# Kernel tuning notes

Measured on AMD Instinct MI355X. Metric: run time of the kernel, lower is better.

Reference implementation:

```python
import jax, jax.numpy as jnp
import numpy as np

B, D, E, G, P, H = 8192, 2048, 8, 4, 512, 192
T, DT, TAU, VTH, VRESET = 20, 0.001, 0.02, 0.5, 0.0
DELTA0, KTOP, KROUTE, PREDW = 7.0, 32, 2, 0.1


def setup_inputs() -> dict:
    key = jax.random.key(0)
    ks = jax.random.split(key, 12)
    s = 0.02
    return {
        "query_embedding": jax.random.normal(ks[0], (B, D), jnp.float32),
        "Wg": jax.random.normal(ks[1], (2, E), jnp.float32) * s,
        "bg": jnp.zeros((E,), jnp.float32),
        "Wp": jax.random.normal(ks[2], (2, E), jnp.float32) * s,
        "bp": jnp.zeros((E,), jnp.float32),
        "Wgg": jax.random.normal(ks[3], (2, G), jnp.float32) * s,
        "bgg": jnp.zeros((G,), jnp.float32),
        "W1": jax.random.normal(ks[4], (E, D, P), jnp.float32) * (1.0 / np.sqrt(D)),
        "b1": jnp.zeros((E, P), jnp.float32),
        "W2": jax.random.normal(ks[5], (E, P, D), jnp.float32) * (1.0 / np.sqrt(P)),
        "b2": jnp.zeros((E, D), jnp.float32),
    }


def reference(query_embedding, Wg, bg, Wp, bp, Wgg, bgg, W1, b1, W2, b2):
    x = query_embedding  # [B, D], already embed_dim -> no pad/slice
    dtype = x.dtype

    # --- Phasor bank temporal features on per-row mean ---
    qm = jnp.mean(x, axis=-1)  # [B]
    freqs = DELTA0 * jnp.arange(1, H + 1, dtype=dtype)  # [H]
    ang = qm[:, None] * freqs[None, :]  # [B, H]
    temporal = jnp.concatenate([jnp.cos(ang), jnp.sin(ang)], axis=-1)  # [B, 2H]

    # --- Spiking attention over top-K |x| indices (LIF over T steps) ---
    topk_idx = jax.lax.top_k(jnp.abs(x), KTOP)[1]  # [B, K]
    rows = jnp.arange(B)[:, None]
    I = jnp.zeros((B, D), dtype).at[rows, topk_idx].add(1.0)  # input current [B, vocab=D]

    def lif_step(v, _):
        v = v * (1.0 - DT / TAU) + I
        spike = (v >= VTH).astype(dtype)
        v = jnp.where(spike > 0, VRESET, v)
        return v, spike

    _, spikes = jax.lax.scan(lif_step, jnp.zeros((B, D), dtype), None, length=T)
    attention_gains = jnp.mean(spikes, axis=0)  # [B, D] spike rates

    # --- Bio gating inputs ---
    gate_in = jnp.stack([jnp.mean(temporal, axis=-1), jnp.mean(attention_gains, axis=-1)], axis=-1)  # [B, 2]

    gate_logits = gate_in @ Wg + bg  # [B, E]
    gate_logits = gate_logits - PREDW * (gate_in @ Wp + bp)

    # group routing bias: experts grouped round-robin i % G
    group_logits = gate_in @ Wgg + bgg  # [B, G]
    gmap = jax.nn.one_hot(jnp.arange(E) % G, G, dtype=dtype)  # [E, G]
    gate_logits = gate_logits + group_logits @ gmap.T

    gate_weights = jax.nn.softmax(gate_logits, axis=-1)  # temperature = 1

    # top-k routing + renormalization
    _, tidx = jax.lax.top_k(gate_weights, KROUTE)
    mask = jnp.zeros_like(gate_weights).at[rows, tidx].set(1.0)
    gated = gate_weights * mask
    gate_weights = gated / (jnp.sum(gated, axis=-1, keepdims=True) + 1e-9)

    # --- Dense MLP experts (bottleneck P = hidden // 4) ---
    h = jax.nn.relu(jnp.einsum('bd,edp->ebp', x, W1) + b1[:, None, :])  # [E, B, P]
    expert_out = jnp.einsum('ebp,eph->ebh', h, W2) + b2[:, None, :]  # [E, B, D]

    # gate-weighted combine
    context = jnp.einsum('be,ebh->bh', gate_weights, expert_out)  # [B, D]
    return context
```

## Files before the change

### kernel.cpp

```cpp
#include <hip/hip_runtime.h>
#include <stdint.h>

#define NB 8192
#define ND 2048
#define NE 8
#define NG 4
#define NP 512
#define NH 192

typedef _Float16 half_t;
typedef half_t f16x8 __attribute__((ext_vector_type(8)));
typedef float f32x4 __attribute__((ext_vector_type(4)));

__device__ __forceinline__ void gload16(const void* g, void* l) {
  __builtin_amdgcn_global_load_lds(
      (const __attribute__((address_space(1))) void*)g,
      (__attribute__((address_space(3))) void*)l, 16, 0, 0);
}

__global__ __launch_bounds__(256) void k_convert(
    const float* __restrict__ x, half_t* __restrict__ xh, double* __restrict__ qm)
{
  const int b = blockIdx.x;
  const int t = threadIdx.x;
  const float* xr = x + (size_t)b * ND;
  const float4 v0 = ((const float4*)xr)[t * 2];
  const float4 v1 = ((const float4*)xr)[t * 2 + 1];
  float f[8] = {v0.x, v0.y, v0.z, v0.w, v1.x, v1.y, v1.z, v1.w};
  double s = 0.0;
  __align__(16) half_t hb[8];
#pragma unroll
  for (int i = 0; i < 8; i++) { s += (double)f[i]; hb[i] = (half_t)f[i]; }
  *reinterpret_cast<int4*>(xh + (size_t)b * ND + t * 8) = *reinterpret_cast<const int4*>(hb);

#pragma unroll
  for (int m = 32; m >= 1; m >>= 1) s += __shfl_xor(s, m);
  __shared__ double part[4];
  if ((t & 63) == 0) part[t >> 6] = s;
  __syncthreads();
  if (t == 0) qm[b] = (part[0] + part[1] + part[2] + part[3]) / (double)ND;
}

__global__ __launch_bounds__(256) void k_gate(
    const double* __restrict__ qm,
    const float* __restrict__ Wg, const float* __restrict__ bg,
    const float* __restrict__ Wp, const float* __restrict__ bp,
    const float* __restrict__ Wgg, const float* __restrict__ bgg,
    int* __restrict__ e0a, int* __restrict__ e1a,
    float* __restrict__ w0a, float* __restrict__ w1a)
{
  const int wave = threadIdx.x >> 6;
  const int lane = threadIdx.x & 63;
  const int b = blockIdx.x * 4 + wave;
  const double q = qm[b];

  double part = 0.0;
#pragma unroll
  for (int i = 0; i < 3; i++) {
    int h = lane + i * 64;
    double ang = q * (7.0 * (double)(h + 1));
    part += cos(ang) + sin(ang);
  }
#pragma unroll
  for (int m = 32; m >= 1; m >>= 1) part += __shfl_xor(part, m);
  const double tm = part / (2.0 * (double)NH);
  const double gi1 = 32.0 / 2048.0;

  double lg = -1.0e300;
  if (lane < 8) {
    const int e = lane, g = e & 3;
    lg = tm * (double)Wg[e] + gi1 * (double)Wg[NE + e] + (double)bg[e];
    lg -= 0.1 * (tm * (double)Wp[e] + gi1 * (double)Wp[NE + e] + (double)bp[e]);
    lg += tm * (double)Wgg[g] + gi1 * (double)Wgg[NG + g] + (double)bgg[g];
  }
  double mx = lg;
#pragma unroll
  for (int m = 4; m >= 1; m >>= 1) mx = fmax(mx, __shfl_xor(mx, m));
  double pe = 0.0;
  if (lane < 8) pe = exp(lg - mx);
  double ps = pe;
#pragma unroll
  for (int m = 4; m >= 1; m >>= 1) ps += __shfl_xor(ps, m);

  double lgs[8], pes[8];
#pragma unroll
  for (int e = 0; e < 8; e++) { lgs[e] = __shfl(lg, e); pes[e] = __shfl(pe, e); }

  if (lane == 0) {
    int e0 = 0;
    for (int e = 1; e < NE; e++) if (lgs[e] > lgs[e0]) e0 = e;
    int e1 = (e0 == 0) ? 1 : 0;
    for (int e = 0; e < NE; e++) if (e != e0 && lgs[e] > lgs[e1]) e1 = e;
    const double p0 = pes[e0] / ps;
    const double p1 = pes[e1] / ps;
    const double den = p0 + p1 + 1e-9;
    e0a[b] = e0; e1a[b] = e1;
    w0a[b] = (float)(p0 / den);
    w1a[b] = (float)(p1 / den);
  }
}

__global__ __launch_bounds__(256) void k_bucket(
    const int* __restrict__ e0a, const int* __restrict__ e1a,
    const float* __restrict__ w0a, const float* __restrict__ w1a,
    int* __restrict__ rowl, float* __restrict__ wl, int* __restrict__ cnt,
    int* __restrict__ pos0a, int* __restrict__ pos1a,
    int* __restrict__ rowlp, int* __restrict__ cntp)
{
  const int t = threadIdx.x;
  const int r = blockIdx.x * 256 + t;
  __shared__ int hist[16], base[16], cursor[16];
  __shared__ int histp[64], basep[64], cursorp[64];
  if (t < 16) { hist[t] = 0; cursor[t] = 0; }
  if (t < 64) { histp[t] = 0; cursorp[t] = 0; }
  __syncthreads();

  const int e0 = e0a[r], e1 = e1a[r];
  const int p = e0 * 8 + e1;
  atomicAdd(&hist[e0], 1);
  atomicAdd(&hist[8 + e1], 1);
  atomicAdd(&histp[p], 1);
  __syncthreads();
  if (t < 16) base[t] = atomicAdd(&cnt[t], hist[t]);
  if (t < 64) basep[t] = atomicAdd(&cntp[t], histp[t]);
  __syncthreads();

  int p0 = atomicAdd(&cursor[e0], 1);
  int idx0 = base[e0] + p0;
  rowl[e0 * NB + idx0] = r;
  wl[e0 * NB + idx0] = w0a[r];
  pos0a[r] = idx0;

  int p1 = atomicAdd(&cursor[8 + e1], 1);
  int idx1 = base[8 + e1] + p1;
  rowl[(8 + e1) * NB + idx1] = r;
  wl[(8 + e1) * NB + idx1] = w1a[r];
  pos1a[r] = idx1;

  int pp = atomicAdd(&cursorp[p], 1);
  rowlp[p * NB + basep[p] + pp] = r;
}

__global__ __launch_bounds__(256) void k_cvt_w(
    const float* __restrict__ W1, const float* __restrict__ W2,
    half_t* __restrict__ w1t, half_t* __restrict__ w2t)
{
  const int which = blockIdx.y;
  const int R = which ? NP : ND;
  const int C = which ? ND : NP;
  const float* src = which ? W2 : W1;
  half_t* dst = which ? w2t : w1t;
  const int tiles_c = C >> 5;
  const int tiles_per_e = (R >> 5) * tiles_c;
  int id = blockIdx.x;
  int e = id / tiles_per_e;
  int rem = id - e * tiles_per_e;
  int tr = rem / tiles_c, tc = rem - tr * tiles_c;
  __shared__ float tile[32][33];
  const int tx = threadIdx.x & 31, ty = threadIdx.x >> 5;
  const float* s = src + (size_t)e * R * C + (size_t)(tr * 32) * C + tc * 32;
#pragma unroll
  for (int i = 0; i < 4; i++)
    tile[ty + i * 8][tx] = s[(size_t)(ty + i * 8) * C + tx];
  __syncthreads();
  half_t* d = dst + (size_t)e * R * C + (size_t)(tc * 32) * R + tr * 32;
#pragma unroll
  for (int i = 0; i < 4; i++)
    d[(size_t)(ty + i * 8) * R + tx] = (half_t)tile[tx][ty + i * 8];
}

__global__ void k_prefix(const int* __restrict__ cnt, const int* __restrict__ cntp,
                         int* __restrict__ pbase,
                         int* __restrict__ i16b, int* __restrict__ i16m, int* __restrict__ n16,
                         int* __restrict__ ipp, int* __restrict__ ipm, int* __restrict__ np)
{
  if (threadIdx.x == 0 && blockIdx.x == 0) {
    int s = 0;
    for (int i = 0; i < 16; i++) { pbase[i] = s; s += cnt[i]; }
    int t = 0;
    for (int b = 0; b < 16; b++)
      for (int m0 = 0; m0 < cnt[b]; m0 += 128) { i16b[t] = b; i16m[t] = m0; t++; }
    *n16 = t;
    t = 0;
    for (int p = 0; p < 64; p++)
      for (int m0 = 0; m0 < cntp[p]; m0 += 128) { ipp[t] = p; ipm[t] = m0; t++; }
    *np = t;
  }
}

__global__ __launch_bounds__(256) void k_gemm1(
    const half_t* __restrict__ xh, const half_t* __restrict__ w1t,
    const float* __restrict__ b1,
    const int* __restrict__ rowl, const float* __restrict__ wl,
    const int* __restrict__ cnt, const int* __restrict__ pbase,
    const int* __restrict__ i16b, const int* __restrict__ i16m,
    const int* __restrict__ n16, half_t* __restrict__ Hbuf)
{
  const int wi = blockIdx.y;
  if (wi >= *n16) return;
  const int bucket = i16b[wi];
  const int m0 = i16m[wi];
  const int count = cnt[bucket];
  const int e = bucket & 7;
  const int n0 = blockIdx.x * 128;
  const int t = threadIdx.x;

  __shared__ __align__(16) half_t As[128 * 32];
  __shared__ __align__(16) half_t Bs[128 * 32];
  __shared__ int rows_s[128];
  __shared__ float ws_s[128];

  if (t < 128) {
    int mi = m0 + t;
    int idx = bucket * NB + (mi < count ? mi : m0);
    rows_s[t] = rowl[idx];
    ws_s[t] = wl[idx];
  }
  __syncthreads();

  const int w = t >> 6, lane = t & 63;
  const int c0 = w * 128 + lane, c1 = c0 + 64;
  const half_t* gA0 = xh + (size_t)rows_s[c0 >> 2] * ND + (c0 & 3) * 8;
  const half_t* gA1 = xh + (size_t)rows_s[c1 >> 2] * ND + (c1 & 3) * 8;
  const half_t* w1te = w1t + (size_t)e * NP * ND;
  const half_t* gB0 = w1te + (size_t)(n0 + (c0 >> 2)) * ND + (c0 & 3) * 8;
  const half_t* gB1 = w1te + (size_t)(n0 + (c1 >> 2)) * ND + (c1 & 3) * 8;
  half_t* lA0 = As + (w * 128) * 8;
  half_t* lA1 = As + (w * 128 + 64) * 8;
  half_t* lB0 = Bs + (w * 128) * 8;
  half_t* lB1 = Bs + (w * 128 + 64) * 8;

  const int wr = w >> 1, wc = w & 1;
  const int lrow = lane & 15, lk = lane >> 4;

  f32x4 acc[4][4];
#pragma unroll
  for (int i = 0; i < 4; i++)
#pragma unroll
    for (int j = 0; j < 4; j++) {
      acc[i][j][0] = 0.f; acc[i][j][1] = 0.f; acc[i][j][2] = 0.f; acc[i][j][3] = 0.f;
    }

  for (int k0 = 0; k0 < ND; k0 += 32) {
    gload16(gA0 + k0, lA0);
    gload16(gA1 + k0, lA1);
    gload16(gB0 + k0, lB0);
    gload16(gB1 + k0, lB1);
    __syncthreads();
    f16x8 af[4], bf[4];
#pragma unroll
    for (int i = 0; i < 4; i++) {
      af[i] = *reinterpret_cast<const f16x8*>(&As[(wr * 64 + i * 16 + lrow) * 32 + lk * 8]);
      bf[i] = *reinterpret_cast<const f16x8*>(&Bs[(wc * 64 + i * 16 + lrow) * 32 + lk * 8]);
    }
#pragma unroll
    for (int mi = 0; mi < 4; mi++)
#pragma unroll
      for (int ni = 0; ni < 4; ni++)
        acc[mi][ni] = __builtin_amdgcn_mfma_f32_16x16x32_f16(af[mi], bf[ni], acc[mi][ni], 0, 0, 0);
    __syncthreads();
  }

  const int pb = pbase[bucket];
#pragma unroll
  for (int mi = 0; mi < 4; mi++) {
#pragma unroll
    for (int i = 0; i < 4; i++) {
      int lm = wr * 64 + mi * 16 + lk * 4 + i;
      if (m0 + lm < count) {
        size_t prow = (size_t)(pb + m0 + lm) * NP;
        float wcoef = ws_s[lm];
#pragma unroll
        for (int ni = 0; ni < 4; ni++) {
          int col = n0 + wc * 64 + ni * 16 + lrow;
          float v = acc[mi][ni][i] + b1[e * NP + col];
          v = v > 0.f ? v : 0.f;
          Hbuf[prow + col] = (half_t)(v * wcoef);
        }
      }
    }
  }
}

__global__ __launch_bounds__(256) void k_gemm2p(
    const half_t* __restrict__ Hbuf, const half_t* __restrict__ w2t,
    const float* __restrict__ b2,
    const int* __restrict__ rowlp, const int* __restrict__ cntp,
    const int* __restrict__ pbase,
    const int* __restrict__ pos0a, const int* __restrict__ pos1a,
    const float* __restrict__ w0a, const float* __restrict__ w1a,
    const int* __restrict__ ipp, const int* __restrict__ ipm,
    const int* __restrict__ np, float* __restrict__ out)
{
  const int wi = blockIdx.y;
  if (wi >= *np) return;
  const int p = ipp[wi];
  const int m0 = ipm[wi];
  const int count = cntp[p];
  const int e0 = p >> 3, e1 = p & 7;
  const int n0 = blockIdx.x * 128;
  const int t = threadIdx.x;

  __shared__ __align__(16) half_t As[128 * 32];
  __shared__ __align__(16) half_t Bs[128 * 32];
  __shared__ int h0_s[128], h1_s[128], rs_s[128];
  __shared__ float w0_s[128], w1_s[128];

  if (t < 128) {
    int mi = m0 + t;
    int r = rowlp[p * NB + (mi < count ? mi : m0)];
    rs_s[t] = r;
    h0_s[t] = pbase[e0] + pos0a[r];
    h1_s[t] = pbase[8 + e1] + pos1a[r];
    w0_s[t] = w0a[r];
    w1_s[t] = w1a[r];
  }
  __syncthreads();

  const int w = t >> 6, lane = t & 63;
  const int c0 = w * 128 + lane, c1 = c0 + 64;
  const half_t* w2e0 = w2t + (size_t)e0 * ND * NP;
  const half_t* w2e1 = w2t + (size_t)e1 * ND * NP;
  const half_t* gB0e0 = w2e0 + (size_t)(n0 + (c0 >> 2)) * NP + (c0 & 3) * 8;
  const half_t* gB1e0 = w2e0 + (size_t)(n0 + (c1 >> 2)) * NP + (c1 & 3) * 8;
  const half_t* gB0e1 = w2e1 + (size_t)(n0 + (c0 >> 2)) * NP + (c0 & 3) * 8;
  const half_t* gB1e1 = w2e1 + (size_t)(n0 + (c1 >> 2)) * NP + (c1 & 3) * 8;
  const half_t* gA0s0 = Hbuf + (size_t)h0_s[c0 >> 2] * NP + (c0 & 3) * 8;
  const half_t* gA1s0 = Hbuf + (size_t)h0_s[c1 >> 2] * NP + (c1 & 3) * 8;
  const half_t* gA0s1 = Hbuf + (size_t)h1_s[c0 >> 2] * NP + (c0 & 3) * 8;
  const half_t* gA1s1 = Hbuf + (size_t)h1_s[c1 >> 2] * NP + (c1 & 3) * 8;
  half_t* lA0 = As + (w * 128) * 8;
  half_t* lA1 = As + (w * 128 + 64) * 8;
  half_t* lB0 = Bs + (w * 128) * 8;
  half_t* lB1 = Bs + (w * 128 + 64) * 8;

  const int wr = w >> 1, wc = w & 1;
  const int lrow = lane & 15, lk = lane >> 4;

  f32x4 acc[4][4];
#pragma unroll
  for (int i = 0; i < 4; i++)
#pragma unroll
    for (int j = 0; j < 4; j++) {
      acc[i][j][0] = 0.f; acc[i][j][1] = 0.f; acc[i][j][2] = 0.f; acc[i][j][3] = 0.f;
    }

  for (int k0 = 0; k0 < NP; k0 += 32) {
    gload16(gA0s0 + k0, lA0);
    gload16(gA1s0 + k0, lA1);
    gload16(gB0e0 + k0, lB0);
    gload16(gB1e0 + k0, lB1);
    __syncthreads();
    f16x8 af[4], bf[4];
#pragma unroll
    for (int i = 0; i < 4; i++) {
      af[i] = *reinterpret_cast<const f16x8*>(&As[(wr * 64 + i * 16 + lrow) * 32 + lk * 8]);
      bf[i] = *reinterpret_cast<const f16x8*>(&Bs[(wc * 64 + i * 16 + lrow) * 32 + lk * 8]);
    }
#pragma unroll
    for (int mi = 0; mi < 4; mi++)
#pragma unroll
      for (int ni = 0; ni < 4; ni++)
        acc[mi][ni] = __builtin_amdgcn_mfma_f32_16x16x32_f16(af[mi], bf[ni], acc[mi][ni], 0, 0, 0);
    __syncthreads();
  }
  for (int k0 = 0; k0 < NP; k0 += 32) {
    gload16(gA0s1 + k0, lA0);
    gload16(gA1s1 + k0, lA1);
    gload16(gB0e1 + k0, lB0);
    gload16(gB1e1 + k0, lB1);
    __syncthreads();
    f16x8 af[4], bf[4];
#pragma unroll
    for (int i = 0; i < 4; i++) {
      af[i] = *reinterpret_cast<const f16x8*>(&As[(wr * 64 + i * 16 + lrow) * 32 + lk * 8]);
      bf[i] = *reinterpret_cast<const f16x8*>(&Bs[(wc * 64 + i * 16 + lrow) * 32 + lk * 8]);
    }
#pragma unroll
    for (int mi = 0; mi < 4; mi++)
#pragma unroll
      for (int ni = 0; ni < 4; ni++)
        acc[mi][ni] = __builtin_amdgcn_mfma_f32_16x16x32_f16(af[mi], bf[ni], acc[mi][ni], 0, 0, 0);
    __syncthreads();
  }

  float b20[4], b21[4];
#pragma unroll
  for (int ni = 0; ni < 4; ni++) {
    int col = n0 + wc * 64 + ni * 16 + lrow;
    b20[ni] = b2[e0 * ND + col];
    b21[ni] = b2[e1 * ND + col];
  }
#pragma unroll
  for (int mi = 0; mi < 4; mi++) {
#pragma unroll
    for (int i = 0; i < 4; i++) {
      int lm = wr * 64 + mi * 16 + lk * 4 + i;
      if (m0 + lm < count) {
        int r = rs_s[lm];
        float wb0 = w0_s[lm], wb1 = w1_s[lm];
        float* orow = out + (size_t)r * ND;
#pragma unroll
        for (int ni = 0; ni < 4; ni++) {
          int col = n0 + wc * 64 + ni * 16 + lrow;
          orow[col] = acc[mi][ni][i] + wb0 * b20[ni] + wb1 * b21[ni];
        }
      }
    }
  }
}

extern "C" void kernel_launch(void* const* d_in, const int* in_sizes, int n_in,
                              void* d_out, int out_size, void* d_ws, size_t ws_size,
                              hipStream_t stream)
{
  const float* x   = (const float*)d_in[0];
  const float* Wg  = (const float*)d_in[1];
  const float* bg  = (const float*)d_in[2];
  const float* Wp  = (const float*)d_in[3];
  const float* bp  = (const float*)d_in[4];
  const float* Wgg = (const float*)d_in[5];
  const float* bgg = (const float*)d_in[6];
  const float* W1  = (const float*)d_in[7];
  const float* b1  = (const float*)d_in[8];
  const float* W2  = (const float*)d_in[9];
  const float* b2  = (const float*)d_in[10];
  float* out = (float*)d_out;

  char* ws = (char*)d_ws;
  size_t off = 0;
  const size_t OFF_XH   = off; off += (size_t)NB * ND * 2;
  const size_t OFF_W1T  = off; off += (size_t)NE * NP * ND * 2;
  const size_t OFF_W2T  = off; off += (size_t)NE * ND * NP * 2;
  const size_t OFF_H    = off; off += (size_t)(2 * NB + 128) * NP * 2;
  const size_t OFF_ROWL = off; off += (size_t)16 * NB * 4;
  const size_t OFF_WL   = off; off += (size_t)16 * NB * 4;
  const size_t OFF_ROWLP= off; off += (size_t)64 * NB * 4;
  const size_t OFF_CNT  = off; off += 64;
  const size_t OFF_CNTP = off; off += 256;
  const size_t OFF_PB   = off; off += 64;
  const size_t OFF_QM   = off; off += (size_t)NB * 8;
  const size_t OFF_E0   = off; off += (size_t)NB * 4;
  const size_t OFF_E1   = off; off += (size_t)NB * 4;
  const size_t OFF_W0   = off; off += (size_t)NB * 4;
  const size_t OFF_W1A  = off; off += (size_t)NB * 4;
  const size_t OFF_POS0 = off; off += (size_t)NB * 4;
  const size_t OFF_POS1 = off; off += (size_t)NB * 4;
  const size_t OFF_I16B = off; off += 1024;
  const size_t OFF_I16M = off; off += 1024;
  const size_t OFF_N16  = off; off += 64;
  const size_t OFF_IPP  = off; off += 1024;
  const size_t OFF_IPM  = off; off += 1024;
  const size_t OFF_NP   = off; off += 64;

  half_t* xh   = (half_t*)(ws + OFF_XH);
  half_t* w1t  = (half_t*)(ws + OFF_W1T);
  half_t* w2t  = (half_t*)(ws + OFF_W2T);
  half_t* Hbuf = (half_t*)(ws + OFF_H);
  int*    rowl = (int*)(ws + OFF_ROWL);
  float*  wl   = (float*)(ws + OFF_WL);
  int*    rowlp= (int*)(ws + OFF_ROWLP);
  int*    cnt  = (int*)(ws + OFF_CNT);
  int*    cntp = (int*)(ws + OFF_CNTP);
  int*    pb   = (int*)(ws + OFF_PB);
  double* qm   = (double*)(ws + OFF_QM);
  int*    e0a  = (int*)(ws + OFF_E0);
  int*    e1a  = (int*)(ws + OFF_E1);
  float*  w0a  = (float*)(ws + OFF_W0);
  float*  w1a  = (float*)(ws + OFF_W1A);
  int*    pos0a= (int*)(ws + OFF_POS0);
  int*    pos1a= (int*)(ws + OFF_POS1);
  int*    i16b = (int*)(ws + OFF_I16B);
  int*    i16m = (int*)(ws + OFF_I16M);
  int*    n16  = (int*)(ws + OFF_N16);
  int*    ipp  = (int*)(ws + OFF_IPP);
  int*    ipm  = (int*)(ws + OFF_IPM);
  int*    np   = (int*)(ws + OFF_NP);

  hipMemsetAsync(cnt, 0, 64 + 256, stream);
  k_convert<<<NB, 256, 0, stream>>>(x, xh, qm);
  k_cvt_w<<<dim3(8192, 2, 1), 256, 0, stream>>>(W1, W2, w1t, w2t);
  k_gate<<<NB / 4, 256, 0, stream>>>(qm, Wg, bg, Wp, bp, Wgg, bgg, e0a, e1a, w0a, w1a);
  k_bucket<<<NB / 256, 256, 0, stream>>>(e0a, e1a, w0a, w1a, rowl, wl, cnt,
                                         pos0a, pos1a, rowlp, cntp);
  k_prefix<<<1, 64, 0, stream>>>(cnt, cntp, pb, i16b, i16m, n16, ipp, ipm, np);
  k_gemm1<<<dim3(4, 144, 1), 256, 0, stream>>>(xh, w1t, b1, rowl, wl, cnt, pb,
                                               i16b, i16m, n16, Hbuf);
  k_gemm2p<<<dim3(16, 128, 1), 256, 0, stream>>>(Hbuf, w2t, b2, rowlp, cntp, pb,
                                                 pos0a, pos1a, w0a, w1a, ipp, ipm, np, out);
}
```

Before: 354.3 us.

## Triple-buffer LDS with async global_load_lds pipeline and XOR swizzle in expert GEMMs

Both grouped expert GEMM kernels now use a 3-stage LDS ring. Tiles are prefetched two iterations ahead with global_load_lds, and explicit vmcnt waits with a single barrier per step replace the two __syncthreads per step. The 16-byte chunks inside each 32-element row are XOR-swizzled by row to cut LDS bank conflicts on the fragment reads, and GEMM2's two expert loops are merged into one 32-step pipeline. In exchange, LDS use per block triples, which may lower occupancy, and the hand-written waitcnt sequencing must be exactly right.

```diff
diff --git a/kernel.cpp b/kernel.cpp
--- a/kernel.cpp
+++ b/kernel.cpp
@@ -205,8 +205,8 @@
   const int n0 = blockIdx.x * 128;
   const int t = threadIdx.x;
 
-  __shared__ __align__(16) half_t As[128 * 32];
-  __shared__ __align__(16) half_t Bs[128 * 32];
+  __shared__ __align__(16) half_t As[3][128 * 32];
+  __shared__ __align__(16) half_t Bs[3][128 * 32];
   __shared__ int rows_s[128];
   __shared__ float ws_s[128];
 
@@ -220,18 +220,18 @@
 
   const int w = t >> 6, lane = t & 63;
   const int c0 = w * 128 + lane, c1 = c0 + 64;
-  const half_t* gA0 = xh + (size_t)rows_s[c0 >> 2] * ND + (c0 & 3) * 8;
-  const half_t* gA1 = xh + (size_t)rows_s[c1 >> 2] * ND + (c1 & 3) * 8;
+  const int row0 = c0 >> 2, ch0 = c0 & 3;
+  const int row1 = c1 >> 2, ch1 = c1 & 3;
+  const int sw0 = (row0 >> 1) & 3, sw1 = (row1 >> 1) & 3;
+  const half_t* gA0 = xh + (size_t)rows_s[row0] * ND + ((ch0 ^ sw0) * 8);
+  const half_t* gA1 = xh + (size_t)rows_s[row1] * ND + ((ch1 ^ sw1) * 8);
   const half_t* w1te = w1t + (size_t)e * NP * ND;
-  const half_t* gB0 = w1te + (size_t)(n0 + (c0 >> 2)) * ND + (c0 & 3) * 8;
-  const half_t* gB1 = w1te + (size_t)(n0 + (c1 >> 2)) * ND + (c1 & 3) * 8;
-  half_t* lA0 = As + (w * 128) * 8;
-  half_t* lA1 = As + (w * 128 + 64) * 8;
-  half_t* lB0 = Bs + (w * 128) * 8;
-  half_t* lB1 = Bs + (w * 128 + 64) * 8;
+  const half_t* gB0 = w1te + (size_t)(n0 + row0) * ND + ((ch0 ^ sw0) * 8);
+  const half_t* gB1 = w1te + (size_t)(n0 + row1) * ND + ((ch1 ^ sw1) * 8);
 
   const int wr = w >> 1, wc = w & 1;
   const int lrow = lane & 15, lk = lane >> 4;
+  const int lko = ((lk ^ ((lrow >> 1) & 3)) * 8);
 
   f32x4 acc[4][4];
 #pragma unroll
@@ -241,24 +241,44 @@
       acc[i][j][0] = 0.f; acc[i][j][1] = 0.f; acc[i][j][2] = 0.f; acc[i][j][3] = 0.f;
     }
 
-  for (int k0 = 0; k0 < ND; k0 += 32) {
-    gload16(gA0 + k0, lA0);
-    gload16(gA1 + k0, lA1);
-    gload16(gB0 + k0, lB0);
-    gload16(gB1 + k0, lB1);
-    __syncthreads();
+  const int NT = ND / 32;
+
+  auto stage = [&](int bi, int tt) {
+    const int kk = tt * 32;
+    half_t* la = &As[bi][w * 1024];
+    half_t* lb = &Bs[bi][w * 1024];
+    gload16(gA0 + kk, la);
+    gload16(gA1 + kk, la + 512);
+    gload16(gB0 + kk, lb);
+    gload16(gB1 + kk, lb + 512);
+  };
+  auto compute = [&](int bi) {
     f16x8 af[4], bf[4];
 #pragma unroll
     for (int i = 0; i < 4; i++) {
-      af[i] = *reinterpret_cast<const f16x8*>(&As[(wr * 64 + i * 16 + lrow) * 32 + lk * 8]);
-      bf[i] = *reinterpret_cast<const f16x8*>(&Bs[(wc * 64 + i * 16 + lrow) * 32 + lk * 8]);
+      af[i] = *reinterpret_cast<const f16x8*>(&As[bi][(wr * 64 + i * 16 + lrow) * 32 + lko]);
+      bf[i] = *reinterpret_cast<const f16x8*>(&Bs[bi][(wc * 64 + i * 16 + lrow) * 32 + lko]);
     }
 #pragma unroll
     for (int mi = 0; mi < 4; mi++)
 #pragma unroll
       for (int ni = 0; ni < 4; ni++)
         acc[mi][ni] = __builtin_amdgcn_mfma_f32_16x16x32_f16(af[mi], bf[ni], acc[mi][ni], 0, 0, 0);
-    __syncthreads();
+  };
+
+  stage(0, 0);
+  stage(1, 1);
+  asm volatile("s_waitcnt vmcnt(4)" ::: "memory");
+  __builtin_amdgcn_s_barrier();
+  for (int tt = 0; tt < NT; ++tt) {
+    asm volatile("" ::: "memory");
+    if (tt + 2 < NT) stage((tt + 2) % 3, tt + 2);
+    compute(tt % 3);
+    if (tt + 1 < NT) {
+      if (tt + 2 < NT) asm volatile("s_waitcnt vmcnt(4) lgkmcnt(0)" ::: "memory");
+      else             asm volatile("s_waitcnt vmcnt(0) lgkmcnt(0)" ::: "memory");
+      __builtin_amdgcn_s_barrier();
+    }
   }
 
   const int pb = pbase[bucket];
@@ -301,8 +321,8 @@
   const int n0 = blockIdx.x * 128;
   const int t = threadIdx.x;
 
-  __shared__ __align__(16) half_t As[128 * 32];
-  __shared__ __align__(16) half_t Bs[128 * 32];
+  __shared__ __align__(16) half_t As[3][128 * 32];
+  __shared__ __align__(16) half_t Bs[3][128 * 32];
   __shared__ int h0_s[128], h1_s[128], rs_s[128];
   __shared__ float w0_s[128], w1_s[128];
 
@@ -319,23 +339,23 @@
 
   const int w = t >> 6, lane = t & 63;
   const int c0 = w * 128 + lane, c1 = c0 + 64;
+  const int row0 = c0 >> 2, ch0 = c0 & 3;
+  const int row1 = c1 >> 2, ch1 = c1 & 3;
+  const int sw0 = (row0 >> 1) & 3, sw1 = (row1 >> 1) & 3;
   const half_t* w2e0 = w2t + (size_t)e0 * ND * NP;
   const half_t* w2e1 = w2t + (size_t)e1 * ND * NP;
-  const half_t* gB0e0 = w2e0 + (size_t)(n0 + (c0 >> 2)) * NP + (c0 & 3) * 8;
-  const half_t* gB1e0 = w2e0 + (size_t)(n0 + (c1 >> 2)) * NP + (c1 & 3) * 8;
-  const half_t* gB0e1 = w2e1 + (size_t)(n0 + (c0 >> 2)) * NP + (c0 & 3) * 8;
-  const half_t* gB1e1 = w2e1 + (size_t)(n0 + (c1 >> 2)) * NP + (c1 & 3) * 8;
-  const half_t* gA0s0 = Hbuf + (size_t)h0_s[c0 >> 2] * NP + (c0 & 3) * 8;
-  const half_t* gA1s0 = Hbuf + (size_t)h0_s[c1 >> 2] * NP + (c1 & 3) * 8;
-  const half_t* gA0s1 = Hbuf + (size_t)h1_s[c0 >> 2] * NP + (c0 & 3) * 8;
-  const half_t* gA1s1 = Hbuf + (size_t)h1_s[c1 >> 2] * NP + (c1 & 3) * 8;
-  half_t* lA0 = As + (w * 128) * 8;
-  half_t* lA1 = As + (w * 128 + 64) * 8;
-  half_t* lB0 = Bs + (w * 128) * 8;
-  half_t* lB1 = Bs + (w * 128 + 64) * 8;
+  const half_t* gA0s0 = Hbuf + (size_t)h0_s[row0] * NP + ((ch0 ^ sw0) * 8);
+  const half_t* gA1s0 = Hbuf + (size_t)h0_s[row1] * NP + ((ch1 ^ sw1) * 8);
+  const half_t* gA0s1 = Hbuf + (size_t)h1_s[row0] * NP + ((ch0 ^ sw0) * 8);
+  const half_t* gA1s1 = Hbuf + (size_t)h1_s[row1] * NP + ((ch1 ^ sw1) * 8);
+  const half_t* gB0e0 = w2e0 + (size_t)(n0 + row0) * NP + ((ch0 ^ sw0) * 8);
+  const half_t* gB1e0 = w2e0 + (size_t)(n0 + row1) * NP + ((ch1 ^ sw1) * 8);
+  const half_t* gB0e1 = w2e1 + (size_t)(n0 + row0) * NP + ((ch0 ^ sw0) * 8);
+  const half_t* gB1e1 = w2e1 + (size_t)(n0 + row1) * NP + ((ch1 ^ sw1) * 8);
 
   const int wr = w >> 1, wc = w & 1;
   const int lrow = lane & 15, lk = lane >> 4;
+  const int lko = ((lk ^ ((lrow >> 1) & 3)) * 8);
 
   f32x4 acc[4][4];
 #pragma unroll
@@ -345,43 +365,51 @@
       acc[i][j][0] = 0.f; acc[i][j][1] = 0.f; acc[i][j][2] = 0.f; acc[i][j][3] = 0.f;
     }
 
-  for (int k0 = 0; k0 < NP; k0 += 32) {
-    gload16(gA0s0 + k0, lA0);
-    gload16(gA1s0 + k0, lA1);
-    gload16(gB0e0 + k0, lB0);
-    gload16(gB1e0 + k0, lB1);
-    __syncthreads();
+  const int NT = 32;
+
+  auto stage = [&](int bi, int tt) {
+    const int kk = (tt & 15) * 32;
+    half_t* la = &As[bi][w * 1024];
+    half_t* lb = &Bs[bi][w * 1024];
+    if (tt & 16) {
+      gload16(gA0s1 + kk, la);
+      gload16(gA1s1 + kk, la + 512);
+      gload16(gB0e1 + kk, lb);
+      gload16(gB1e1 + kk, lb + 512);
+    } else {
+      gload16(gA0s0 + kk, la);
+      gload16(gA1s0 + kk, la + 512);
+      gload16(gB0e0 + kk, lb);
+      gload16(gB1e0 + kk, lb + 512);
+    }
+  };
+  auto compute = [&](int bi) {
     f16x8 af[4], bf[4];
 #pragma unroll
     for (int i = 0; i < 4; i++) {
-      af[i] = *reinterpret_cast<const f16x8*>(&As[(wr * 64 + i * 16 + lrow) * 32 + lk * 8]);
-      bf[i] = *reinterpret_cast<const f16x8*>(&Bs[(wc * 64 + i * 16 + lrow) * 32 + lk * 8]);
+      af[i] = *reinterpret_cast<const f16x8*>(&As[bi][(wr * 64 + i * 16 + lrow) * 32 + lko]);
+      bf[i] = *reinterpret_cast<const f16x8*>(&Bs[bi][(wc * 64 + i * 16 + lrow) * 32 + lko]);
     }
 #pragma unroll
     for (int mi = 0; mi < 4; mi++)
 #pragma unroll
       for (int ni = 0; ni < 4; ni++)
         acc[mi][ni] = __builtin_amdgcn_mfma_f32_16x16x32_f16(af[mi], bf[ni], acc[mi][ni], 0, 0, 0);
-    __syncthreads();
-  }
-  for (int k0 = 0; k0 < NP; k0 += 32) {
-    gload16(gA0s1 + k0, lA0);
-    gload16(gA1s1 + k0, lA1);
-    gload16(gB0e1 + k0, lB0);
-    gload16(gB1e1 + k0, lB1);
-    __syncthreads();
-    f16x8 af[4], bf[4];
-#pragma unroll
-    for (int i = 0; i < 4; i++) {
-      af[i] = *reinterpret_cast<const f16x8*>(&As[(wr * 64 + i * 16 + lrow) * 32 + lk * 8]);
-      bf[i] = *reinterpret_cast<const f16x8*>(&Bs[(wc * 64 + i * 16 + lrow) * 32 + lk * 8]);
-    }
-#pragma unroll
-    for (int mi = 0; mi < 4; mi++)
-#pragma unroll
-      for (int ni = 0; ni < 4; ni++)
-        acc[mi][ni] = __builtin_amdgcn_mfma_f32_16x16x32_f16(af[mi], bf[ni], acc[mi][ni], 0, 0, 0);
-    __syncthreads();
+  };
+
+  stage(0, 0);
+  stage(1, 1);
+  asm volatile("s_waitcnt vmcnt(4)" ::: "memory");
+  __builtin_amdgcn_s_barrier();
+  for (int tt = 0; tt < NT; ++tt) {
+    asm volatile("" ::: "memory");
+    if (tt + 2 < NT) stage((tt + 2) % 3, tt + 2);
+    compute(tt % 3);
+    if (tt + 1 < NT) {
+      if (tt + 2 < NT) asm volatile("s_waitcnt vmcnt(4) lgkmcnt(0)" ::: "memory");
+      else             asm volatile("s_waitcnt vmcnt(0) lgkmcnt(0)" ::: "memory");
+      __builtin_amdgcn_s_barrier();
+    }
   }
 
   float b20[4], b21[4];
```

Result: no change. 357.1 us (+0.8%).
